# Kernel optimization log

Hardware: AMD Instinct MI355X
Metric: run time of the kernel (lower is better)

Reference implementation:

```python
import jax, jax.numpy as jnp
import numpy as np
from jax import lax

# dims (see shape_source)
V, E = 100000, 200        # vocab, embedding dim
HID = 256; H = HID // 2    # BiLSTM hidden, per-direction
K = 24                     # tagset size (incl START/STOP)
B, T = 64, 1024
START, STOP = 0, 1
NEG = -10000.0


def setup_inputs() -> dict:
    key = jax.random.key(0)
    ks = jax.random.split(key, 16)
    s = 0.1  # init scale to keep LSTM gates in a sane range
    return {
        "sentences": jax.random.randint(ks[0], (B, T), 0, V, dtype=jnp.int32),
        "lens": jnp.full((B,), T, dtype=jnp.int32),
        "emb": jax.random.normal(ks[1], (V, E), dtype=jnp.float32) * s,
        # PyTorch LSTM layout: W_ih [4H, in], W_hh [4H, H], gate order i,f,g,o
        "W_ih_f": jax.random.normal(ks[2], (4 * H, E)) * s,
        "W_hh_f": jax.random.normal(ks[3], (4 * H, H)) * s,
        "b_ih_f": jax.random.normal(ks[4], (4 * H,)) * s,
        "b_hh_f": jax.random.normal(ks[5], (4 * H,)) * s,
        "W_ih_b": jax.random.normal(ks[6], (4 * H, E)) * s,
        "W_hh_b": jax.random.normal(ks[7], (4 * H, H)) * s,
        "b_ih_b": jax.random.normal(ks[8], (4 * H,)) * s,
        "b_hh_b": jax.random.normal(ks[9], (4 * H,)) * s,
        # init_hidden(): random h0/c0, [2 directions, B, H]
        "h0": jax.random.normal(ks[10], (2, B, H)),
        "c0": jax.random.normal(ks[11], (2, B, H)),
        # hidden2tag: nn.Linear(hidden_dim, K) -> weight [K, HID]
        "W_out": jax.random.normal(ks[12], (K, HID)) * s,
        "b_out": jax.random.normal(ks[13], (K,)) * s,
        "transitions": jax.random.normal(ks[14], (K, K)),  # [to, from]
    }


def _lstm_dir(x, W_ih, W_hh, b_ih, b_hh, h0, c0):
    """x: [T, B, in] -> hs: [T, B, H]. PyTorch LSTM cell math."""
    def step(carry, xt):
        h, c = carry
        g = xt @ W_ih.T + b_ih + h @ W_hh.T + b_hh  # [B, 4H]
        i, f, gg, o = jnp.split(g, 4, axis=-1)
        i = jax.nn.sigmoid(i); f = jax.nn.sigmoid(f)
        gg = jnp.tanh(gg); o = jax.nn.sigmoid(o)
        c = f * c + i * gg
        h = o * jnp.tanh(c)
        return (h, c), h
    _, hs = lax.scan(step, (h0, c0), x)
    return hs


def _viterbi_batch(feats, transitions):
    """feats: [B, T, K]. Batched version of _viterbi_decode.
    Returns (path_score [B], best_path [B, T])."""
    b = feats.shape[0]
    v0 = jnp.full((b, K), NEG, feats.dtype).at[:, START].set(0.0)
    transT = transitions.T  # [prev, next]

    def step(v, feat_t):
        # scores[b, prev, next] = v[b, prev] + trans(next <- prev)
        scores = v[:, :, None] + transT[None, :, :]
        best = jnp.max(scores, axis=1)          # [B, K]
        bptr = jnp.argmax(scores, axis=1)       # [B, K] best prev per next
        return best + feat_t, bptr

    v, bptrs = lax.scan(step, v0, jnp.swapaxes(feats, 0, 1))  # bptrs [T, B, K]
    terminal = v + transitions[STOP][None, :]
    path_score = jnp.max(terminal, axis=1)      # [B]
    last_tag = jnp.argmax(terminal, axis=1)     # [B]

    def back(tag, bp):
        prev = jnp.take_along_axis(bp, tag[:, None], axis=1)[:, 0]
        return prev, tag

    _, path = lax.scan(back, last_tag, bptrs, reverse=True)  # [T, B]
    return path_score, path.T


def reference(sentences, lens, emb, W_ih_f, W_hh_f, b_ih_f, b_hh_f,
              W_ih_b, W_hh_b, b_ih_b, b_hh_b, h0, c0, W_out, b_out,
              transitions):
    # embedding lookup; forward() packs raw w_embeds (dropout branch unused)
    x = emb[sentences]                       # [B, T, E]
    x = jnp.swapaxes(x, 0, 1)                # [T, B, E] (time-major like LSTM)
    hf = _lstm_dir(x, W_ih_f, W_hh_f, b_ih_f, b_hh_f, h0[0], c0[0])
    hb = _lstm_dir(x[::-1], W_ih_b, W_hh_b, b_ih_b, b_hh_b, h0[1], c0[1])[::-1]
    out = jnp.concatenate([hf, hb], axis=-1)  # [T, B, HID]
    feats = out @ W_out.T + b_out             # [T, B, K]
    feats = jnp.swapaxes(feats, 0, 1)          # [B, T, K]
    # all lens == T, so per-sentence slicing is the full sequence
    path_score, tag_seqs = _viterbi_batch(feats, transitions)
    return path_score, tag_seqs
```

## Files before the change

kernel.cpp:

```cpp
#include <hip/hip_runtime.h>
#include <math.h>

#define Ee   200
#define Hh   128
#define G4   512
#define Kk   24
#define Bb   64
#define Tt   1024
#define HIDd 256
#define NEGf (-10000.0f)
#define PSTR 9

__global__ __launch_bounds__(256) void k_wt(const float* __restrict__ Wf,
                                            const float* __restrict__ Wb,
                                            float* __restrict__ Wt) {
    int idx = blockIdx.x * 256 + threadIdx.x;
    if (idx >= Ee * 1024) return;
    int k = idx >> 10, n = idx & 1023;
    Wt[idx] = (n < G4) ? Wf[n * Ee + k] : Wb[(n - G4) * Ee + k];
}

__global__ __launch_bounds__(256, 2) void k_gemm3(const int* __restrict__ sent,
                                                  const float* __restrict__ emb,
                                                  const float* __restrict__ Wt,
                                                  float* __restrict__ Uc,
                                                  int c0T, int CT, int unified) {
    __shared__ float As[2][8][128];
    __shared__ float Bs[2][8][256];
    __shared__ int   toks[128];

    int tid = threadIdx.x;
    int n0  = blockIdx.x * 256;
    int m0  = blockIdx.y * 128;
    int dz  = blockIdx.z;
    int ty  = tid >> 4, tx = tid & 15;

    if (tid < 128) {
        int m = m0 + tid;
        int it = m >> 6, b = m & 63;
        int t = unified ? it : (dz ? (Tt - 1 - (c0T + it)) : (c0T + it));
        toks[tid] = sent[b * Tt + t];
    }
    __syncthreads();

    int am = tid & 127, ak4 = tid >> 7;
    int brow = tid >> 5, bc4 = tid & 31;

    const float* aptr = emb + (size_t)toks[am] * Ee + ak4 * 4;
    int bcol0 = (unified ? 0 : dz * G4) + n0;
    const float* bptr = Wt + (size_t)brow * 1024 + bcol0 + bc4 * 4;

    float acc[8][16];
#pragma unroll
    for (int i = 0; i < 8; ++i)
#pragma unroll
        for (int j = 0; j < 16; ++j) acc[i][j] = 0.f;

    float4 av  = *(const float4*)(aptr);
    float4 bv0 = *(const float4*)(bptr);
    float4 bv1 = *(const float4*)(bptr + 128);

    const int NK = Ee / 8;
    for (int k = 0; k < NK; ++k) {
        int cur = k & 1;
        As[cur][ak4 * 4 + 0][am] = av.x;
        As[cur][ak4 * 4 + 1][am] = av.y;
        As[cur][ak4 * 4 + 2][am] = av.z;
        As[cur][ak4 * 4 + 3][am] = av.w;
        *(float4*)&Bs[cur][brow][bc4 * 4]       = bv0;
        *(float4*)&Bs[cur][brow][128 + bc4 * 4] = bv1;
        __syncthreads();

        if (k + 1 < NK) {
            int kc = (k + 1) * 8;
            av  = *(const float4*)(aptr + kc);
            bv0 = *(const float4*)(bptr + (size_t)kc * 1024);
            bv1 = *(const float4*)(bptr + (size_t)kc * 1024 + 128);
        }

#pragma unroll
        for (int kk = 0; kk < 8; ++kk) {
            float a_[8], b_[16];
            *(float4*)&a_[0] = *(const float4*)&As[cur][kk][ty * 8];
            *(float4*)&a_[4] = *(const float4*)&As[cur][kk][ty * 8 + 4];
#pragma unroll
            for (int q = 0; q < 4; ++q)
                *(float4*)&b_[4 * q] = *(const float4*)&Bs[cur][kk][tx * 4 + 64 * q];
#pragma unroll
            for (int i = 0; i < 8; ++i)
#pragma unroll
                for (int j = 0; j < 16; ++j)
                    acc[i][j] = fmaf(a_[i], b_[j], acc[i][j]);
        }
    }

    int dd   = unified ? (n0 >> 9) : dz;
    int ncol = unified ? (n0 & 511) : n0;
    float* base = Uc + (size_t)dd * ((size_t)CT * Bb * G4);
#pragma unroll
    for (int i = 0; i < 8; ++i) {
        float* dst = base + (size_t)(m0 + ty * 8 + i) * G4 + ncol + tx * 4;
#pragma unroll
        for (int q = 0; q < 4; ++q)
            *(float4*)(dst + 64 * q) = make_float4(acc[i][4 * q], acc[i][4 * q + 1],
                                                   acc[i][4 * q + 2], acc[i][4 * q + 3]);
    }
}

__global__ __launch_bounds__(512, 2) void k_lstm2(const float* __restrict__ Uc,
                                                  const float* __restrict__ Whh_f,
                                                  const float* __restrict__ Whh_b,
                                                  const float* __restrict__ bih_f,
                                                  const float* __restrict__ bhh_f,
                                                  const float* __restrict__ bih_b,
                                                  const float* __restrict__ bhh_b,
                                                  const float* __restrict__ h0v,
                                                  const float* __restrict__ c0v,
                                                  const float* __restrict__ Wout,
                                                  float* __restrict__ hst,
                                                  float* __restrict__ cst,
                                                  float* __restrict__ pf,
                                                  int c0T, int CT, int first, int unified) {
    __shared__ float hsh[Hh];
    __shared__ float gsh[G4];
    __shared__ float ps[(G4 + Kk) * PSTR];

    int tid  = threadIdx.x;
    int lane = tid & 63, wv = tid >> 6;
    int b = blockIdx.x & 63, d = blockIdx.x >> 6;

    const float* Whh = d ? Whh_b : Whh_f;
    float bias = d ? (bih_b[tid] + bhh_b[tid]) : (bih_f[tid] + bhh_f[tid]);

    float w[8][16];
#pragma unroll
    for (int ri = 0; ri < 8; ++ri) {
        const float* wr = Whh + (size_t)(ri * 64 + lane) * Hh + wv * 16;
#pragma unroll
        for (int c4 = 0; c4 < 4; ++c4)
            *(float4*)&w[ri][c4 * 4] = *(const float4*)(wr + c4 * 4);
    }
    float wt[16];
    if (lane < Kk) {
        const float* wr = Wout + (size_t)lane * HIDd + d * Hh + wv * 16;
#pragma unroll
        for (int c4 = 0; c4 < 4; ++c4)
            *(float4*)&wt[c4 * 4] = *(const float4*)(wr + c4 * 4);
    }

    float cc = 0.f;
    if (tid < Hh) {
        int si = (d * Bb + b) * Hh + tid;
        hsh[tid] = first ? h0v[si] : hst[si];
        cc       = first ? c0v[si] : cst[si];
    }
    __syncthreads();

    const float* Ub = Uc + (size_t)d * ((size_t)CT * Bb * G4);
    int u0 = unified ? (d ? (Tt - 1) : 0) : 0;
    int us = unified ? (d ? -1 : 1) : 1;

    float ucur = Ub[(size_t)u0 * (Bb * G4) + b * G4 + tid];
    float unext = 0.f;

    for (int i = 0; i <= CT; ++i) {
        int last = (i == CT);
        float hv[16];
        *(float4*)&hv[0]  = *(const float4*)&hsh[wv * 16];
        *(float4*)&hv[4]  = *(const float4*)&hsh[wv * 16 + 4];
        *(float4*)&hv[8]  = *(const float4*)&hsh[wv * 16 + 8];
        *(float4*)&hv[12] = *(const float4*)&hsh[wv * 16 + 12];

        if (lane < Kk) {
            float s = 0.f;
#pragma unroll
            for (int c = 0; c < 16; ++c) s = fmaf(wt[c], hv[c], s);
            ps[(G4 + lane) * PSTR + wv] = s;
        }
        if (!last) {
#pragma unroll
            for (int ri = 0; ri < 8; ++ri) {
                float s = 0.f;
#pragma unroll
                for (int c = 0; c < 16; ++c) s = fmaf(w[ri][c], hv[c], s);
                ps[(ri * 64 + lane) * PSTR + wv] = s;
            }
            if (i + 1 < CT)
                unext = Ub[(size_t)(u0 + (i + 1) * us) * (Bb * G4) + b * G4 + tid];
        }
        __syncthreads();

        if (!last) {
            const float* pr = ps + (size_t)tid * PSTR;
            float s = ((pr[0] + pr[1]) + (pr[2] + pr[3])) +
                      ((pr[4] + pr[5]) + (pr[6] + pr[7]));
            s += ucur + bias;
            int gt = tid >> 7;
            gsh[tid] = (gt == 2) ? tanhf(s) : 1.f / (1.f + expf(-s));
        }
        __syncthreads();

        if (!last && tid < Hh) {
            float gi = gsh[tid], gf = gsh[Hh + tid];
            float gg = gsh[2 * Hh + tid], go = gsh[3 * Hh + tid];
            cc = gf * cc + gi * gg;
            hsh[tid] = go * tanhf(cc);
        }
        if (tid >= 128 && tid < 128 + Kk && i >= 1) {
            int k = tid - 128;
            const float* pr = ps + (size_t)(G4 + k) * PSTR;
            float s = ((pr[0] + pr[1]) + (pr[2] + pr[3])) +
                      ((pr[4] + pr[5]) + (pr[6] + pr[7]));
            int tp = c0T + i - 1;
            int tg = d ? (Tt - 1 - tp) : tp;
            pf[((size_t)(d * Bb + b) * Tt + tg) * Kk + k] = s;
        }
        __syncthreads();
        ucur = unext;
    }

    if (tid < Hh) {
        int si = (d * Bb + b) * Hh + tid;
        hst[si] = hsh[tid];
        cst[si] = cc;
    }
}

#define CMB(av, ai, bv_, bi_, ov, oi)                         \
    { bool g = (bv_) > (av); ov = g ? (bv_) : (av); oi = g ? (bi_) : (ai); }

__global__ __launch_bounds__(64) void k_viterbi(const float* __restrict__ pf,
                                                const float* __restrict__ bout,
                                                const float* __restrict__ trans,
                                                float* __restrict__ out) {
    __shared__ unsigned char bptr[Tt * Kk];
    __shared__ float fsh[2][64][25];
    __shared__ float tsh[Kk];
    __shared__ unsigned char path[Tt];

    int lane = threadIdx.x;
    int b    = blockIdx.x;
    int half   = (lane >= Kk) ? 1 : 0;
    int n      = half ? (lane - Kk) : lane;
    int active = (lane < 2 * Kk);

    float tr[12];
    float bo = 0.f;
    if (active) {
#pragma unroll
        for (int j = 0; j < 12; ++j) tr[j] = trans[n * Kk + half * 12 + j];
        bo = bout[n];
    }
    float v = (lane == 0) ? 0.f : NEGf;

    const float* p0 = pf + (size_t)b * Tt * Kk;
    const float* p1 = pf + (size_t)(Bb + b) * Tt * Kk;

    float4 r0[6], r1[6];
#pragma unroll
    for (int j = 0; j < 6; ++j) {
        int f = 4 * (lane + 64 * j);
        r0[j] = *(const float4*)(p0 + f);
        r1[j] = *(const float4*)(p1 + f);
    }
#pragma unroll
    for (int j = 0; j < 6; ++j) {
        int f = 4 * (lane + 64 * j);
        int s = f / 24, k = f - 24 * s;
        fsh[0][s][k + 0] = r0[j].x + r1[j].x;
        fsh[0][s][k + 1] = r0[j].y + r1[j].y;
        fsh[0][s][k + 2] = r0[j].z + r1[j].z;
        fsh[0][s][k + 3] = r0[j].w + r1[j].w;
    }

    for (int c = 0; c < 16; ++c) {
        int cur = c & 1;
        if (c + 1 < 16) {
            const float* q0 = p0 + (c + 1) * 1536;
            const float* q1 = p1 + (c + 1) * 1536;
#pragma unroll
            for (int j = 0; j < 6; ++j) {
                int f = 4 * (lane + 64 * j);
                r0[j] = *(const float4*)(q0 + f);
                r1[j] = *(const float4*)(q1 + f);
            }
        }

        for (int s = 0; s < 64; ++s) {
            int t = c * 64 + s;
            if (active) {
                int pb = half * 12;
                float sc[12];
#pragma unroll
                for (int j = 0; j < 12; ++j) sc[j] = __shfl(v, pb + j) + tr[j];

                float l1v[6]; int l1i[6];
#pragma unroll
                for (int j = 0; j < 6; ++j)
                    CMB(sc[2 * j], 2 * j, sc[2 * j + 1], 2 * j + 1, l1v[j], l1i[j]);
                float l2v[3]; int l2i[3];
#pragma unroll
                for (int j = 0; j < 3; ++j)
                    CMB(l1v[2 * j], l1i[2 * j], l1v[2 * j + 1], l1i[2 * j + 1],
                        l2v[j], l2i[j]);
                float dv; int di;
                CMB(l2v[0], l2i[0], l2v[1], l2i[1], dv, di);
                float best; int bp;
                CMB(dv, di, l2v[2], l2i[2], best, bp);
                bp += pb;

                float ob  = __shfl(best, n + Kk);
                int   obp = __shfl(bp,   n + Kk);
                if (half == 0) {
                    if (ob > best) { best = ob; bp = obp; }
                    v = best + fsh[cur][s][n] + bo;
                    bptr[t * Kk + n] = (unsigned char)bp;
                }
            }
        }

        if (c + 1 < 16) {
#pragma unroll
            for (int j = 0; j < 6; ++j) {
                int f = 4 * (lane + 64 * j);
                int s = f / 24, k = f - 24 * s;
                fsh[cur ^ 1][s][k + 0] = r0[j].x + r1[j].x;
                fsh[cur ^ 1][s][k + 1] = r0[j].y + r1[j].y;
                fsh[cur ^ 1][s][k + 2] = r0[j].z + r1[j].z;
                fsh[cur ^ 1][s][k + 3] = r0[j].w + r1[j].w;
            }
        }
    }

    if (half == 0 && lane < Kk) tsh[n] = v + trans[1 * Kk + n];
    __syncthreads();

    if (lane == 0) {
        float bestv = tsh[0];
        int tag = 0;
        for (int q = 1; q < Kk; ++q)
            if (tsh[q] > bestv) { bestv = tsh[q]; tag = q; }
        out[b] = bestv;
        for (int t = Tt - 1; t >= 1; --t) {
            path[t] = (unsigned char)tag;
            tag = bptr[t * Kk + tag];
        }
        path[0] = (unsigned char)tag;
    }
    __syncthreads();

    float* otag = out + Bb + (size_t)b * Tt;
    for (int t = lane; t < Tt; t += 64) otag[t] = (float)path[t];
}

extern "C" void kernel_launch(void* const* d_in, const int* in_sizes, int n_in,
                              void* d_out, int out_size, void* d_ws, size_t ws_size,
                              hipStream_t stream) {
    const int*   sent  = (const int*)d_in[0];
    const float* emb   = (const float*)d_in[2];
    const float* Wih_f = (const float*)d_in[3];
    const float* Whh_f = (const float*)d_in[4];
    const float* bih_f = (const float*)d_in[5];
    const float* bhh_f = (const float*)d_in[6];
    const float* Wih_b = (const float*)d_in[7];
    const float* Whh_b = (const float*)d_in[8];
    const float* bih_b = (const float*)d_in[9];
    const float* bhh_b = (const float*)d_in[10];
    const float* h0    = (const float*)d_in[11];
    const float* c0    = (const float*)d_in[12];
    const float* Wout  = (const float*)d_in[13];
    const float* bout  = (const float*)d_in[14];
    const float* trans = (const float*)d_in[15];

    float* ws  = (float*)d_ws;
    float* Wt  = ws;
    float* pf  = Wt + 204800;
    float* hst = pf + 3145728;
    float* cst = hst + 16384;
    float* Uc  = cst + 16384;

    const size_t fixedf = 204800 + 3145728 + 16384 + 16384;
    size_t needU = (size_t)2 * Tt * Bb * G4;
    int unified = ((fixedf + needU) * 4 <= ws_size);

    k_wt<<<(Ee * 1024 + 255) / 256, 256, 0, stream>>>(Wih_f, Wih_b, Wt);

    if (unified) {
        k_gemm3<<<dim3(4, 512, 1), 256, 0, stream>>>(sent, emb, Wt, Uc, 0, Tt, 1);
        k_lstm2<<<128, 512, 0, stream>>>(Uc, Whh_f, Whh_b, bih_f, bhh_f,
                                         bih_b, bhh_b, h0, c0, Wout,
                                         hst, cst, pf, 0, Tt, 1, 1);
    } else {
        int CT = 64;
        const int cands[3] = {512, 256, 128};
        for (int ci = 0; ci < 3; ++ci)
            if ((fixedf + (size_t)2 * cands[ci] * Bb * G4) * 4 <= ws_size) {
                CT = cands[ci]; break;
            }
        int NC = Tt / CT;
        for (int cix = 0; cix < NC; ++cix) {
            k_gemm3<<<dim3(2, CT * 64 / 128, 2), 256, 0, stream>>>(
                sent, emb, Wt, Uc, cix * CT, CT, 0);
            k_lstm2<<<128, 512, 0, stream>>>(Uc, Whh_f, Whh_b, bih_f, bhh_f,
                                             bih_b, bhh_b, h0, c0, Wout,
                                             hst, cst, pf, cix * CT, CT,
                                             cix == 0, 0);
        }
    }

    k_viterbi<<<Bb, 64, 0, stream>>>(pf, bout, trans, (float*)d_out);
}
```

Measured before the change: 1.520 ms.

## Overlap input-projection GEMM for next chunk with LSTM recurrence in combined kernel

The full-sequence path now splits time into chunks of 256 steps. Each chunk runs one combined launch in which 128 blocks do the LSTM recurrence for the current chunk while the extra blocks compute the input-projection GEMM for the next chunk. The aim is to hide GEMM time behind the latency-bound recurrence instead of running a large GEMM before it. This adds launches, per-chunk reloading of weights and h/c state, and the larger shared-memory footprint of the combined kernel, which could limit occupancy.

After: 1.409 ms. 1.08x faster.

```diff
diff --git a/kernel.cpp b/kernel.cpp
--- a/kernel.cpp
+++ b/kernel.cpp
@@ -10,6 +10,7 @@
 #define HIDd 256
 #define NEGf (-10000.0f)
 #define PSTR 9
+#define CTC  256
 
 __global__ __launch_bounds__(256) void k_wt(const float* __restrict__ Wf,
                                             const float* __restrict__ Wb,
@@ -20,117 +21,110 @@
     Wt[idx] = (n < G4) ? Wf[n * Ee + k] : Wb[(n - G4) * Ee + k];
 }
 
-__global__ __launch_bounds__(256, 2) void k_gemm3(const int* __restrict__ sent,
-                                                  const float* __restrict__ emb,
-                                                  const float* __restrict__ Wt,
-                                                  float* __restrict__ Uc,
-                                                  int c0T, int CT, int unified) {
-    __shared__ float As[2][8][128];
-    __shared__ float Bs[2][8][256];
-    __shared__ int   toks[128];
-
-    int tid = threadIdx.x;
-    int n0  = blockIdx.x * 256;
-    int m0  = blockIdx.y * 128;
-    int dz  = blockIdx.z;
-    int ty  = tid >> 4, tx = tid & 15;
+__device__ __forceinline__ void gemm_tile(const int* __restrict__ sent,
+                                          const float* __restrict__ emb,
+                                          const float* __restrict__ Wt,
+                                          float* __restrict__ Uc,
+                                          int m0, int n0, int tid,
+                                          float* As, float* Bs, int* toks) {
+    bool act = (tid < 256);
+    int ty = (tid & 255) >> 4, tx = tid & 15;
 
     if (tid < 128) {
         int m = m0 + tid;
-        int it = m >> 6, b = m & 63;
-        int t = unified ? it : (dz ? (Tt - 1 - (c0T + it)) : (c0T + it));
-        toks[tid] = sent[b * Tt + t];
+        toks[tid] = sent[(m & 63) * Tt + (m >> 6)];
     }
     __syncthreads();
 
-    int am = tid & 127, ak4 = tid >> 7;
-    int brow = tid >> 5, bc4 = tid & 31;
-
-    const float* aptr = emb + (size_t)toks[am] * Ee + ak4 * 4;
-    int bcol0 = (unified ? 0 : dz * G4) + n0;
-    const float* bptr = Wt + (size_t)brow * 1024 + bcol0 + bc4 * 4;
-
+    int am = tid & 127, ak4 = (tid >> 7) & 1;
+    int brow = (tid >> 5) & 7, bc4 = tid & 31;
+
+    const float* aptr = emb;
+    const float* bptr = Wt;
+    float4 av = make_float4(0, 0, 0, 0), bv0 = av, bv1 = av;
     float acc[8][16];
-#pragma unroll
-    for (int i = 0; i < 8; ++i)
-#pragma unroll
-        for (int j = 0; j < 16; ++j) acc[i][j] = 0.f;
-
-    float4 av  = *(const float4*)(aptr);
-    float4 bv0 = *(const float4*)(bptr);
-    float4 bv1 = *(const float4*)(bptr + 128);
+    if (act) {
+        aptr = emb + (size_t)toks[am] * Ee + ak4 * 4;
+        bptr = Wt + (size_t)brow * 1024 + n0 + bc4 * 4;
+#pragma unroll
+        for (int i = 0; i < 8; ++i)
+#pragma unroll
+            for (int j = 0; j < 16; ++j) acc[i][j] = 0.f;
+        av  = *(const float4*)(aptr);
+        bv0 = *(const float4*)(bptr);
+        bv1 = *(const float4*)(bptr + 128);
+    }
 
     const int NK = Ee / 8;
     for (int k = 0; k < NK; ++k) {
         int cur = k & 1;
-        As[cur][ak4 * 4 + 0][am] = av.x;
-        As[cur][ak4 * 4 + 1][am] = av.y;
-        As[cur][ak4 * 4 + 2][am] = av.z;
-        As[cur][ak4 * 4 + 3][am] = av.w;
-        *(float4*)&Bs[cur][brow][bc4 * 4]       = bv0;
-        *(float4*)&Bs[cur][brow][128 + bc4 * 4] = bv1;
+        if (act) {
+            As[cur * 1024 + (ak4 * 4 + 0) * 128 + am] = av.x;
+            As[cur * 1024 + (ak4 * 4 + 1) * 128 + am] = av.y;
+            As[cur * 1024 + (ak4 * 4 + 2) * 128 + am] = av.z;
+            As[cur * 1024 + (ak4 * 4 + 3) * 128 + am] = av.w;
+            *(float4*)&Bs[cur * 2048 + brow * 256 + bc4 * 4]       = bv0;
+            *(float4*)&Bs[cur * 2048 + brow * 256 + 128 + bc4 * 4] = bv1;
+        }
         __syncthreads();
 
-        if (k + 1 < NK) {
+        if (act && k + 1 < NK) {
             int kc = (k + 1) * 8;
             av  = *(const float4*)(aptr + kc);
             bv0 = *(const float4*)(bptr + (size_t)kc * 1024);
             bv1 = *(const float4*)(bptr + (size_t)kc * 1024 + 128);
         }
 
-#pragma unroll
-        for (int kk = 0; kk < 8; ++kk) {
-            float a_[8], b_[16];
-            *(float4*)&a_[0] = *(const float4*)&As[cur][kk][ty * 8];
-            *(float4*)&a_[4] = *(const float4*)&As[cur][kk][ty * 8 + 4];
+        if (act) {
+#pragma unroll
+            for (int kk = 0; kk < 8; ++kk) {
+                float a_[8], b_[16];
+                *(float4*)&a_[0] = *(const float4*)&As[cur * 1024 + kk * 128 + ty * 8];
+                *(float4*)&a_[4] = *(const float4*)&As[cur * 1024 + kk * 128 + ty * 8 + 4];
+#pragma unroll
+                for (int q = 0; q < 4; ++q)
+                    *(float4*)&b_[4 * q] =
+                        *(const float4*)&Bs[cur * 2048 + kk * 256 + tx * 4 + 64 * q];
+#pragma unroll
+                for (int i = 0; i < 8; ++i)
+#pragma unroll
+                    for (int j = 0; j < 16; ++j)
+                        acc[i][j] = fmaf(a_[i], b_[j], acc[i][j]);
+            }
+        }
+    }
+
+    if (act) {
+        int dd = n0 >> 9, ncol = n0 & 511;
+        float* base = Uc + (size_t)dd * ((size_t)Tt * Bb * G4);
+#pragma unroll
+        for (int i = 0; i < 8; ++i) {
+            float* dst = base + (size_t)(m0 + ty * 8 + i) * G4 + ncol + tx * 4;
 #pragma unroll
             for (int q = 0; q < 4; ++q)
-                *(float4*)&b_[4 * q] = *(const float4*)&Bs[cur][kk][tx * 4 + 64 * q];
-#pragma unroll
-            for (int i = 0; i < 8; ++i)
-#pragma unroll
-                for (int j = 0; j < 16; ++j)
-                    acc[i][j] = fmaf(a_[i], b_[j], acc[i][j]);
-        }
-    }
-
-    int dd   = unified ? (n0 >> 9) : dz;
-    int ncol = unified ? (n0 & 511) : n0;
-    float* base = Uc + (size_t)dd * ((size_t)CT * Bb * G4);
-#pragma unroll
-    for (int i = 0; i < 8; ++i) {
-        float* dst = base + (size_t)(m0 + ty * 8 + i) * G4 + ncol + tx * 4;
-#pragma unroll
-        for (int q = 0; q < 4; ++q)
-            *(float4*)(dst + 64 * q) = make_float4(acc[i][4 * q], acc[i][4 * q + 1],
-                                                   acc[i][4 * q + 2], acc[i][4 * q + 3]);
-    }
-}
-
-__global__ __launch_bounds__(512, 2) void k_lstm2(const float* __restrict__ Uc,
-                                                  const float* __restrict__ Whh_f,
-                                                  const float* __restrict__ Whh_b,
-                                                  const float* __restrict__ bih_f,
-                                                  const float* __restrict__ bhh_f,
-                                                  const float* __restrict__ bih_b,
-                                                  const float* __restrict__ bhh_b,
-                                                  const float* __restrict__ h0v,
-                                                  const float* __restrict__ c0v,
-                                                  const float* __restrict__ Wout,
-                                                  float* __restrict__ hst,
-                                                  float* __restrict__ cst,
-                                                  float* __restrict__ pf,
-                                                  int c0T, int CT, int first, int unified) {
-    __shared__ float hsh[Hh];
-    __shared__ float gsh[G4];
-    __shared__ float ps[(G4 + Kk) * PSTR];
-
-    int tid  = threadIdx.x;
+                *(float4*)(dst + 64 * q) =
+                    make_float4(acc[i][4 * q], acc[i][4 * q + 1],
+                                acc[i][4 * q + 2], acc[i][4 * q + 3]);
+        }
+    }
+}
+
+__device__ __forceinline__ void lstm_chunk(const float* __restrict__ Uc,
+                                           const float* __restrict__ Whh,
+                                           const float* __restrict__ bih,
+                                           const float* __restrict__ bhh,
+                                           const float* __restrict__ h0v,
+                                           const float* __restrict__ c0v,
+                                           const float* __restrict__ Wout,
+                                           float* __restrict__ hst,
+                                           float* __restrict__ cst,
+                                           float* __restrict__ pf,
+                                           int b, int d, int c0T, int CT,
+                                           int first, int unified, int tid,
+                                           float* hsh, float* gsh, float* ps) {
     int lane = tid & 63, wv = tid >> 6;
-    int b = blockIdx.x & 63, d = blockIdx.x >> 6;
-
-    const float* Whh = d ? Whh_b : Whh_f;
-    float bias = d ? (bih_b[tid] + bhh_b[tid]) : (bih_f[tid] + bhh_f[tid]);
+
+    float bias = bih[tid] + bhh[tid];
 
     float w[8][16];
 #pragma unroll
@@ -156,8 +150,8 @@
     }
     __syncthreads();
 
-    const float* Ub = Uc + (size_t)d * ((size_t)CT * Bb * G4);
-    int u0 = unified ? (d ? (Tt - 1) : 0) : 0;
+    const float* Ub = Uc + (size_t)d * ((size_t)(unified ? Tt : CT) * Bb * G4);
+    int u0 = unified ? (d ? (Tt - 1 - c0T) : c0T) : 0;
     int us = unified ? (d ? -1 : 1) : 1;
 
     float ucur = Ub[(size_t)u0 * (Bb * G4) + b * G4 + tid];
@@ -224,6 +218,156 @@
         hst[si] = hsh[tid];
         cst[si] = cc;
     }
+}
+
+__global__ __launch_bounds__(256, 2) void k_gpro(const int* __restrict__ sent,
+                                                 const float* __restrict__ emb,
+                                                 const float* __restrict__ Wt,
+                                                 float* __restrict__ Uc,
+                                                 int nc0, int CT) {
+    __shared__ float As[2048];
+    __shared__ float Bs[4096];
+    __shared__ int   toks[128];
+    int gid = blockIdx.x;
+    int band = gid / CT, rem = gid % CT;
+    int ni = rem & 1, mi = rem >> 1;
+    int m0 = (band ? (Tt - nc0 - CT) : nc0) * 64 + mi * 128;
+    int n0 = band * 512 + ni * 256;
+    gemm_tile(sent, emb, Wt, Uc, m0, n0, threadIdx.x, As, Bs, toks);
+}
+
+__global__ __launch_bounds__(512) void k_combo(const int* __restrict__ sent,
+                                               const float* __restrict__ emb,
+                                               const float* __restrict__ Wt,
+                                               float* __restrict__ Uc,
+                                               const float* __restrict__ Whh_f,
+                                               const float* __restrict__ Whh_b,
+                                               const float* __restrict__ bih_f,
+                                               const float* __restrict__ bhh_f,
+                                               const float* __restrict__ bih_b,
+                                               const float* __restrict__ bhh_b,
+                                               const float* __restrict__ h0,
+                                               const float* __restrict__ c0,
+                                               const float* __restrict__ Wout,
+                                               float* __restrict__ hst,
+                                               float* __restrict__ cst,
+                                               float* __restrict__ pf,
+                                               int c0T, int first, int nc0) {
+    __shared__ float smem[35840];
+    int bid = blockIdx.x;
+    if (bid < 128) {
+        int b = bid & 63, d = bid >> 6;
+        lstm_chunk(Uc, d ? Whh_b : Whh_f, d ? bih_b : bih_f, d ? bhh_b : bhh_f,
+                   h0, c0, Wout, hst, cst, pf, b, d, c0T, CTC, first, 1,
+                   threadIdx.x, smem, smem + 128, smem + 640);
+    } else {
+        int gid = bid - 128;
+        int band = gid / CTC, rem = gid % CTC;
+        int ni = rem & 1, mi = rem >> 1;
+        int m0 = (band ? (Tt - nc0 - CTC) : nc0) * 64 + mi * 128;
+        int n0 = band * 512 + ni * 256;
+        gemm_tile(sent, emb, Wt, Uc, m0, n0, threadIdx.x,
+                  smem, smem + 2048, (int*)(smem + 6144));
+    }
+}
+
+__global__ __launch_bounds__(256, 2) void k_gemm3(const int* __restrict__ sent,
+                                                  const float* __restrict__ emb,
+                                                  const float* __restrict__ Wt,
+                                                  float* __restrict__ Uc,
+                                                  int c0T, int CT) {
+    __shared__ float As[2048];
+    __shared__ float Bs[4096];
+    __shared__ int   toks[128];
+    int n0 = blockIdx.x * 256 + blockIdx.z * G4;
+    int dz = blockIdx.z;
+    int m0 = blockIdx.y * 128;
+    bool act = true;
+    int tid = threadIdx.x;
+    if (tid < 128) {
+        int m = m0 + tid;
+        int it = m >> 6, b = m & 63;
+        int t = dz ? (Tt - 1 - (c0T + it)) : (c0T + it);
+        toks[tid] = sent[b * Tt + t];
+    }
+    __syncthreads();
+    int ty = tid >> 4, tx = tid & 15;
+    int am = tid & 127, ak4 = tid >> 7;
+    int brow = tid >> 5, bc4 = tid & 31;
+    const float* aptr = emb + (size_t)toks[am] * Ee + ak4 * 4;
+    const float* bptr = Wt + (size_t)brow * 1024 + n0 + bc4 * 4;
+    float acc[8][16];
+#pragma unroll
+    for (int i = 0; i < 8; ++i)
+#pragma unroll
+        for (int j = 0; j < 16; ++j) acc[i][j] = 0.f;
+    float4 av  = *(const float4*)(aptr);
+    float4 bv0 = *(const float4*)(bptr);
+    float4 bv1 = *(const float4*)(bptr + 128);
+    const int NK = Ee / 8;
+    for (int k = 0; k < NK; ++k) {
+        int cur = k & 1;
+        As[cur * 1024 + (ak4 * 4 + 0) * 128 + am] = av.x;
+        As[cur * 1024 + (ak4 * 4 + 1) * 128 + am] = av.y;
+        As[cur * 1024 + (ak4 * 4 + 2) * 128 + am] = av.z;
+        As[cur * 1024 + (ak4 * 4 + 3) * 128 + am] = av.w;
+        *(float4*)&Bs[cur * 2048 + brow * 256 + bc4 * 4]       = bv0;
+        *(float4*)&Bs[cur * 2048 + brow * 256 + 128 + bc4 * 4] = bv1;
+        __syncthreads();
+        if (k + 1 < NK) {
+            int kc = (k + 1) * 8;
+            av  = *(const float4*)(aptr + kc);
+            bv0 = *(const float4*)(bptr + (size_t)kc * 1024);
+            bv1 = *(const float4*)(bptr + (size_t)kc * 1024 + 128);
+        }
+#pragma unroll
+        for (int kk = 0; kk < 8; ++kk) {
+            float a_[8], b_[16];
+            *(float4*)&a_[0] = *(const float4*)&As[cur * 1024 + kk * 128 + ty * 8];
+            *(float4*)&a_[4] = *(const float4*)&As[cur * 1024 + kk * 128 + ty * 8 + 4];
+#pragma unroll
+            for (int q = 0; q < 4; ++q)
+                *(float4*)&b_[4 * q] =
+                    *(const float4*)&Bs[cur * 2048 + kk * 256 + tx * 4 + 64 * q];
+#pragma unroll
+            for (int i = 0; i < 8; ++i)
+#pragma unroll
+                for (int j = 0; j < 16; ++j)
+                    acc[i][j] = fmaf(a_[i], b_[j], acc[i][j]);
+        }
+    }
+    float* base = Uc + (size_t)dz * ((size_t)CT * Bb * G4);
+    int ncol = blockIdx.x * 256;
+#pragma unroll
+    for (int i = 0; i < 8; ++i) {
+        float* dst = base + (size_t)(m0 + ty * 8 + i) * G4 + ncol + tx * 4;
+#pragma unroll
+        for (int q = 0; q < 4; ++q)
+            *(float4*)(dst + 64 * q) = make_float4(acc[i][4 * q], acc[i][4 * q + 1],
+                                                   acc[i][4 * q + 2], acc[i][4 * q + 3]);
+    }
+    (void)act;
+}
+
+__global__ __launch_bounds__(512, 2) void k_lstm2(const float* __restrict__ Uc,
+                                                  const float* __restrict__ Whh_f,
+                                                  const float* __restrict__ Whh_b,
+                                                  const float* __restrict__ bih_f,
+                                                  const float* __restrict__ bhh_f,
+                                                  const float* __restrict__ bih_b,
+                                                  const float* __restrict__ bhh_b,
+                                                  const float* __restrict__ h0,
+                                                  const float* __restrict__ c0,
+                                                  const float* __restrict__ Wout,
+                                                  float* __restrict__ hst,
+                                                  float* __restrict__ cst,
+                                                  float* __restrict__ pf,
+                                                  int c0T, int CT, int first) {
+    __shared__ float smem[5464];
+    int b = blockIdx.x & 63, d = blockIdx.x >> 6;
+    lstm_chunk(Uc, d ? Whh_b : Whh_f, d ? bih_b : bih_f, d ? bhh_b : bhh_f,
+               h0, c0, Wout, hst, cst, pf, b, d, c0T, CT, first, 0,
+               threadIdx.x, smem, smem + 128, smem + 640);
 }
 
 #define CMB(av, ai, bv_, bi_, ov, oi)                         \
@@ -386,10 +530,17 @@
     k_wt<<<(Ee * 1024 + 255) / 256, 256, 0, stream>>>(Wih_f, Wih_b, Wt);
 
     if (unified) {
-        k_gemm3<<<dim3(4, 512, 1), 256, 0, stream>>>(sent, emb, Wt, Uc, 0, Tt, 1);
-        k_lstm2<<<128, 512, 0, stream>>>(Uc, Whh_f, Whh_b, bih_f, bhh_f,
-                                         bih_b, bhh_b, h0, c0, Wout,
-                                         hst, cst, pf, 0, Tt, 1, 1);
+        const int NC = Tt / CTC;
+        k_gpro<<<2 * CTC, 256, 0, stream>>>(sent, emb, Wt, Uc, 0, CTC);
+        for (int c = 0; c < NC; ++c) {
+            int hasg = (c + 1 < NC);
+            int grid = 128 + (hasg ? 2 * CTC : 0);
+            k_combo<<<grid, 512, 0, stream>>>(sent, emb, Wt, Uc,
+                                              Whh_f, Whh_b, bih_f, bhh_f,
+                                              bih_b, bhh_b, h0, c0, Wout,
+                                              hst, cst, pf,
+                                              c * CTC, c == 0, (c + 1) * CTC);
+        }
     } else {
         int CT = 64;
         const int cands[3] = {512, 256, 128};
@@ -400,11 +551,11 @@
         int NC = Tt / CT;
         for (int cix = 0; cix < NC; ++cix) {
             k_gemm3<<<dim3(2, CT * 64 / 128, 2), 256, 0, stream>>>(
-                sent, emb, Wt, Uc, cix * CT, CT, 0);
+                sent, emb, Wt, Uc, cix * CT, CT);
             k_lstm2<<<128, 512, 0, stream>>>(Uc, Whh_f, Whh_b, bih_f, bhh_f,
                                              bih_b, bhh_b, h0, c0, Wout,
                                              hst, cst, pf, cix * CT, CT,
-                                             cix == 0, 0);
+                                             cix == 0);
         }
     }
 
```
